# Kernel optimization log

Measured on AMD Instinct MI355X. Metric: run time of the kernel, lower is better.

The kernel has to match this reference:

```python
import jax, jax.numpy as jnp
import numpy as np

NUM_EXPERTS = 8
TOP_K = 2


def setup_inputs() -> dict:
    key = jax.random.key(0)
    ks = jax.random.split(key, 5)
    B, S, H, F, E = 2, 2048, 1024, 4096, NUM_EXPERTS
    return {
        "hidden_states": jax.random.normal(ks[0], (B, S, H), dtype=jnp.float32),
        "router_w": jax.random.normal(ks[1], (H, E), dtype=jnp.float32) * 0.02,
        "router_b": jnp.zeros((E,), dtype=jnp.float32),
        "w1": jax.random.normal(ks[2], (E, H, F), dtype=jnp.float32) * 0.02,
        "b1": jnp.zeros((E, F), dtype=jnp.float32),
        "w2": jax.random.normal(ks[3], (E, F, H), dtype=jnp.float32) * 0.02,
        "b2": jnp.zeros((E, H), dtype=jnp.float32),
    }


def reference(hidden_states, router_w, router_b, w1, b1, w2, b2):
    # Router: softmax over experts, take top-2, renormalize.
    logits = jnp.einsum("bsh,he->bse", hidden_states, router_w) + router_b
    probs = jax.nn.softmax(logits, axis=-1)
    top_w, top_i = jax.lax.top_k(probs, TOP_K)              # [B,S,2]
    top_w = top_w / jnp.sum(top_w, axis=-1, keepdims=True)
    # Combine weights per expert: [B,S,E] (sum of slot weights where routed).
    combine = jnp.sum(
        top_w[..., None] * jax.nn.one_hot(top_i, NUM_EXPERTS, dtype=top_w.dtype),
        axis=-2,
    )
    # Dense expert FFN over stacked experts (grouped GEMM form).
    h = jax.nn.gelu(
        jnp.einsum("bsh,ehf->ebsf", hidden_states, w1) + b1[:, None, None, :],
        approximate=False,
    )  # exact GELU matches torch nn.GELU default
    y = jnp.einsum("ebsf,efh->ebsh", h, w2) + b2[:, None, None, :]
    # Weighted combine of top-2 expert outputs per token.
    return jnp.einsum("bse,ebsh->bsh", combine, y)
```

## Files before the change

kernel.cpp:

```cpp
#include <hip/hip_runtime.h>
#include <hip/hip_bf16.h>
#include <stdint.h>

#define T_TOKENS 4096
#define H_DIM    1024
#define F_DIM    4096
#define NE       8
#define NA       8192

typedef __bf16 bf16x8 __attribute__((ext_vector_type(8)));
typedef float  f32x4  __attribute__((ext_vector_type(4)));

__device__ __forceinline__ float b2f(unsigned short u) {
    union { float f; uint32_t i; } v; v.i = ((uint32_t)u) << 16; return v.f;
}
__device__ __forceinline__ unsigned short f2b(float f) {
    union { float f; uint32_t i; } v; v.f = f;
    uint32_t x = v.i;
    return (unsigned short)((x + 0x7FFFu + ((x >> 16) & 1u)) >> 16);
}

__device__ __forceinline__ float gelu_f(float x) {
    float z = fabsf(x) * 0.70710678118f;
    float t = 1.0f / (1.0f + 0.3275911f * z);
    float p = t * (0.254829592f + t * (-0.284496736f +
              t * (1.421413741f + t * (-1.453152027f + t * 1.061405429f))));
    float erf_z = 1.0f - p * __expf(-z * z);
    float sgn_erf = (x >= 0.f) ? erf_z : -erf_z;
    return x * (0.5f + 0.5f * sgn_erf);
}

__device__ __forceinline__ void gl_lds16(const void* g, void* l) {
    __builtin_amdgcn_global_load_lds(
        (const __attribute__((address_space(1))) void*)g,
        (__attribute__((address_space(3))) void*)l,
        16, 0, 0);
}

__global__ void probe_kernel(const unsigned short* __restrict__ hs,
                             int* __restrict__ flag) {
    int lane = threadIdx.x;
    int cnt = 0;
    for (int j = 0; j < 16; j++) {
        unsigned short u = hs[(lane * 16 + j) * 2];
        int e = (u >> 7) & 0xFF;
        if (e >= 100 && e <= 135) cnt++;
    }
    for (int off = 32; off > 0; off >>= 1) cnt += __shfl_down(cnt, off);
    if (lane == 0) *flag = (cnt >= 512) ? 0 : 1;
}

__global__ __launch_bounds__(256) void router_kernel(
    const void* __restrict__ hs, const void* __restrict__ rw,
    const void* __restrict__ rb, const int* __restrict__ flag,
    int* __restrict__ top_i, float* __restrict__ top_w,
    unsigned short* __restrict__ hsb) {
    bool f32 = (*flag != 0);
    int wave = threadIdx.x >> 6, lane = threadIdx.x & 63;
    int t = blockIdx.x * 4 + wave;
    unsigned short* hout = hsb + (size_t)t * H_DIM;
    float acc[NE];
#pragma unroll
    for (int e = 0; e < NE; e++) acc[e] = 0.f;
    if (f32) {
        const float* hrow = (const float*)hs + (size_t)t * H_DIM;
        const float* rwf = (const float*)rw;
        for (int j = 0; j < 16; j++) {
            int k = j * 64 + lane;
            float h = hrow[k];
            hout[k] = f2b(h);
            float4 a = *(const float4*)(rwf + (size_t)k * NE);
            float4 b = *(const float4*)(rwf + (size_t)k * NE + 4);
            acc[0] += h * a.x; acc[1] += h * a.y; acc[2] += h * a.z; acc[3] += h * a.w;
            acc[4] += h * b.x; acc[5] += h * b.y; acc[6] += h * b.z; acc[7] += h * b.w;
        }
    } else {
        const unsigned short* hrow = (const unsigned short*)hs + (size_t)t * H_DIM;
        const unsigned short* rwu = (const unsigned short*)rw;
        for (int j = 0; j < 16; j++) {
            int k = j * 64 + lane;
            unsigned short hu = hrow[k];
            hout[k] = hu;
            float h = b2f(hu);
            uint4 rv = *(const uint4*)(rwu + (size_t)k * NE);
            const unsigned short* rs = (const unsigned short*)&rv;
#pragma unroll
            for (int e = 0; e < NE; e++) acc[e] += h * b2f(rs[e]);
        }
    }
#pragma unroll
    for (int e = 0; e < NE; e++)
        for (int off = 32; off > 0; off >>= 1) acc[e] += __shfl_down(acc[e], off);
    if (lane == 0) {
        float lg[NE];
#pragma unroll
        for (int e = 0; e < NE; e++)
            lg[e] = acc[e] + (f32 ? ((const float*)rb)[e]
                                  : b2f(((const unsigned short*)rb)[e]));
        int e0 = 0;
        for (int e = 1; e < NE; e++) if (lg[e] > lg[e0]) e0 = e;
        int e1 = (e0 == 0) ? 1 : 0;
        for (int e = 0; e < NE; e++) if (e != e0 && lg[e] > lg[e1]) e1 = e;
        float w0 = 1.f / (1.f + expf(lg[e1] - lg[e0]));
        top_i[t * 2] = e0; top_i[t * 2 + 1] = e1;
        top_w[t * 2] = w0; top_w[t * 2 + 1] = 1.f - w0;
    }
}

__global__ __launch_bounds__(256) void assign_kernel(
    const int* __restrict__ top_i, const float* __restrict__ top_w,
    int* __restrict__ token_list, float* __restrict__ wgt_list,
    int* __restrict__ assign_row, int* __restrict__ counts,
    int* __restrict__ offsets) {
    __shared__ int cnt_s[NE], cur_s[NE];
    int tid = threadIdx.x;
    if (tid < NE) cnt_s[tid] = 0;
    __syncthreads();
    for (int idx = tid; idx < NA; idx += 256) atomicAdd(&cnt_s[top_i[idx]], 1);
    __syncthreads();
    if (tid == 0) {
        int run = 0;
        for (int e = 0; e < NE; e++) {
            offsets[e] = run; counts[e] = cnt_s[e]; cur_s[e] = run; run += cnt_s[e];
        }
    }
    __syncthreads();
    for (int idx = tid; idx < NA; idx += 256) {
        int e = top_i[idx];
        int pos = atomicAdd(&cur_s[e], 1);
        token_list[pos] = idx >> 1;
        wgt_list[pos] = top_w[idx];
        assign_row[idx] = pos;
    }
}

__global__ __launch_bounds__(256) void transpose_kernel(
    const void* __restrict__ in, unsigned short* __restrict__ out,
    int R, int C, const int* __restrict__ flag) {
    bool f32 = (*flag != 0);
    size_t zo = (size_t)blockIdx.z * R * C;
    int c0 = blockIdx.x * 64, r0 = blockIdx.y * 64;
    __shared__ unsigned short t[64][65];
    int tx = threadIdx.x & 15, ty = threadIdx.x >> 4;
    if (f32) {
        const float* inf = (const float*)in + zo;
#pragma unroll
        for (int i = 0; i < 4; i++) {
            int r = ty + i * 16;
            float4 v = *(const float4*)&inf[(size_t)(r0 + r) * C + c0 + tx * 4];
            t[r][tx * 4] = f2b(v.x); t[r][tx * 4 + 1] = f2b(v.y);
            t[r][tx * 4 + 2] = f2b(v.z); t[r][tx * 4 + 3] = f2b(v.w);
        }
    } else {
        const unsigned short* inu = (const unsigned short*)in + zo;
#pragma unroll
        for (int i = 0; i < 4; i++) {
            int r = ty + i * 16;
            ushort4 v = *(const ushort4*)&inu[(size_t)(r0 + r) * C + c0 + tx * 4];
            t[r][tx * 4] = v.x; t[r][tx * 4 + 1] = v.y;
            t[r][tx * 4 + 2] = v.z; t[r][tx * 4 + 3] = v.w;
        }
    }
    __syncthreads();
#pragma unroll
    for (int i = 0; i < 4; i++) {
        int cc = ty + i * 16;
        ushort4 w;
        w.x = t[tx * 4][cc]; w.y = t[tx * 4 + 1][cc];
        w.z = t[tx * 4 + 2][cc]; w.w = t[tx * 4 + 3][cc];
        *(ushort4*)&out[zo + (size_t)(c0 + cc) * R + r0 + tx * 4] = w;
    }
}

template <int MODE>
__global__ __launch_bounds__(512, 2) void gemm_kernel(
    const unsigned short* __restrict__ Abase,
    const unsigned short* __restrict__ Bt,
    const void* __restrict__ bias,
    const int* __restrict__ flag,
    const int* __restrict__ token_list, const float* __restrict__ wgt_list,
    const int* __restrict__ counts, const int* __restrict__ offsets,
    unsigned short* __restrict__ act_out, unsigned short* __restrict__ y_out) {
    constexpr int K    = (MODE == 0) ? H_DIM : F_DIM;
    constexpr int NDIM = (MODE == 0) ? F_DIM : H_DIM;
    constexpr int AST  = K;
    constexpr int BM   = 256;
    constexpr int BN   = (MODE == 0) ? 256 : 128;
    constexpr int WM   = (MODE == 0) ? 2 : 4;
    constexpr int WN   = (MODE == 0) ? 4 : 2;
    constexpr int MI   = BM / (16 * WM);
    constexpr int NJ   = BN / (16 * WN);
    constexpr int NK   = K / 32;
    constexpr int ABUF = BM * 32;
    constexpr int BBUF = BN * 32;
    constexpr int NIA  = BM / 128;
    constexpr int NIB  = BN / 128;

    const int lid = blockIdx.x + gridDim.x * (blockIdx.y + gridDim.y * blockIdx.z);
    const int e   = lid & 7;
    const int r_  = lid >> 3;
    const int nx  = r_ % gridDim.x;
    const int my  = r_ / gridDim.x;

    const int cnt = counts[e];
    const int m0 = my * BM;
    if (m0 >= cnt) return;
    const int off = offsets[e];
    const int n0 = nx * BN;
    const bool f32 = (*flag != 0);

    __shared__ __bf16 As[2 * ABUF];
    __shared__ __bf16 Bs[2 * BBUF];
    __shared__ int   tok_s[BM];
    __shared__ float wgt_s[BM];

    const int tid = threadIdx.x;
    const int wave = tid >> 6, lane = tid & 63;

    if (tid < BM) {
        int r = off + min(m0 + tid, cnt - 1);
        tok_s[tid] = (MODE == 0) ? token_list[r] : r;
        wgt_s[tid] = wgt_list[r];
    }
    __syncthreads();

    const char* Abytes = (const char*)Abase;
    const char* Bbytes = (const char*)(Bt + (size_t)e * NDIM * K);
    const int rl = lane >> 2;
    const int chk = (lane & 3) ^ (rl & 3);
    uint64_t ga[NIA], gb[NIB];
    uint32_t la[NIA], lb[NIB];
#pragma unroll
    for (int j = 0; j < NIA; j++) {
        int rowA = (wave * NIA + j) * 16 + rl;
        ga[j] = (uint64_t)(uintptr_t)(Abytes + ((size_t)tok_s[rowA] * AST + chk * 8) * 2);
        la[j] = (wave * NIA + j) * 512;
    }
#pragma unroll
    for (int j = 0; j < NIB; j++) {
        int rowB = n0 + (wave * NIB + j) * 16 + rl;
        gb[j] = (uint64_t)(uintptr_t)(Bbytes + ((size_t)rowB * K + chk * 8) * 2);
        lb[j] = (wave * NIB + j) * 512;
    }

    f32x4 acc[MI][NJ];
#pragma unroll
    for (int i = 0; i < MI; i++)
#pragma unroll
        for (int j = 0; j < NJ; j++) acc[i][j] = (f32x4){0.f, 0.f, 0.f, 0.f};

    const int wr = wave / WN, wc = wave % WN;
    const int lane15 = lane & 15, quad = lane >> 4;

#pragma unroll
    for (int j = 0; j < NIA; j++) {
        gl_lds16((const void*)(uintptr_t)ga[j], (void*)(As + la[j]));
        ga[j] += 64;
    }
#pragma unroll
    for (int j = 0; j < NIB; j++) {
        gl_lds16((const void*)(uintptr_t)gb[j], (void*)(Bs + lb[j]));
        gb[j] += 64;
    }
    __syncthreads();

    for (int kt = 0; kt < NK; kt++) {
        const int cur = kt & 1;
        if (kt + 1 < NK) {
            const int nxt = cur ^ 1;
#pragma unroll
            for (int j = 0; j < NIA; j++) {
                gl_lds16((const void*)(uintptr_t)ga[j], (void*)(As + nxt * ABUF + la[j]));
                ga[j] += 64;
            }
#pragma unroll
            for (int j = 0; j < NIB; j++) {
                gl_lds16((const void*)(uintptr_t)gb[j], (void*)(Bs + nxt * BBUF + lb[j]));
                gb[j] += 64;
            }
        }
        const __bf16* Ab = As + cur * ABUF;
        const __bf16* Bb = Bs + cur * BBUF;
        bf16x8 a[MI], b[NJ];
#pragma unroll
        for (int i = 0; i < MI; i++) {
            int row = wr * (BM / WM) + i * 16 + lane15;
            a[i] = *(const bf16x8*)&Ab[row * 32 + ((quad ^ (row & 3)) * 8)];
        }
#pragma unroll
        for (int j = 0; j < NJ; j++) {
            int row = wc * (BN / WN) + j * 16 + lane15;
            b[j] = *(const bf16x8*)&Bb[row * 32 + ((quad ^ (row & 3)) * 8)];
        }
#pragma unroll
        for (int i = 0; i < MI; i++)
#pragma unroll
            for (int j = 0; j < NJ; j++)
                acc[i][j] = __builtin_amdgcn_mfma_f32_16x16x32_bf16(a[i], b[j], acc[i][j], 0, 0, 0);
        __syncthreads();
    }

#pragma unroll
    for (int j = 0; j < NJ; j++) {
        int col = n0 + wc * (BN / WN) + j * 16 + lane15;
        float bv = f32 ? ((const float*)bias)[(size_t)e * NDIM + col]
                       : b2f(((const unsigned short*)bias)[(size_t)e * NDIM + col]);
#pragma unroll
        for (int i = 0; i < MI; i++) {
#pragma unroll
            for (int r = 0; r < 4; r++) {
                int rowl = wr * (BM / WM) + i * 16 + quad * 4 + r;
                if (m0 + rowl < cnt) {
                    float v = acc[i][j][r] + bv;
                    if (MODE == 0) {
                        act_out[(size_t)(off + m0 + rowl) * F_DIM + col] = f2b(gelu_f(v));
                    } else {
                        y_out[(size_t)(off + m0 + rowl) * H_DIM + col] = f2b(v * wgt_s[rowl]);
                    }
                }
            }
        }
    }
}

__global__ __launch_bounds__(256) void combine_kernel(
    const unsigned short* __restrict__ y, const int* __restrict__ assign_row,
    void* __restrict__ out, const int* __restrict__ flag) {
    bool f32 = (*flag != 0);
    int t = blockIdx.x;
    int r0 = assign_row[t * 2], r1 = assign_row[t * 2 + 1];
    ushort4 a = ((const ushort4*)(y + (size_t)r0 * H_DIM))[threadIdx.x];
    ushort4 b = ((const ushort4*)(y + (size_t)r1 * H_DIM))[threadIdx.x];
    float s0 = b2f(a.x) + b2f(b.x), s1 = b2f(a.y) + b2f(b.y);
    float s2 = b2f(a.z) + b2f(b.z), s3 = b2f(a.w) + b2f(b.w);
    if (f32) {
        float4 o = {s0, s1, s2, s3};
        ((float4*)out)[(size_t)t * (H_DIM / 4) + threadIdx.x] = o;
    } else {
        ushort4 o;
        o.x = f2b(s0); o.y = f2b(s1); o.z = f2b(s2); o.w = f2b(s3);
        ((ushort4*)((unsigned short*)out + (size_t)t * H_DIM))[threadIdx.x] = o;
    }
}

extern "C" void kernel_launch(void* const* d_in, const int* in_sizes, int n_in,
                              void* d_out, int out_size, void* d_ws, size_t ws_size,
                              hipStream_t stream) {
    const void* hs = d_in[0];
    const void* rw = d_in[1];
    const void* rb = d_in[2];
    const void* w1 = d_in[3];
    const void* b1 = d_in[4];
    const void* w2 = d_in[5];
    const void* b2 = d_in[6];

    char* ws = (char*)d_ws;
    size_t o = 0;
    auto alloc = [&](size_t bytes) {
        char* p = ws + o; o += (bytes + 255) & ~(size_t)255; return p;
    };
    unsigned short* wt   = (unsigned short*)alloc((size_t)NE * F_DIM * H_DIM * 2);
    unsigned short* act  = (unsigned short*)alloc((size_t)NA * F_DIM * 2);
    unsigned short* yb   = (unsigned short*)alloc((size_t)NA * H_DIM * 2);
    unsigned short* hsb  = (unsigned short*)alloc((size_t)T_TOKENS * H_DIM * 2);
    int*   top_i      = (int*)alloc(NA * 4);
    float* top_w      = (float*)alloc(NA * 4);
    int*   token_list = (int*)alloc(NA * 4);
    float* wgt_list   = (float*)alloc(NA * 4);
    int*   assign_row = (int*)alloc(NA * 4);
    int*   counts     = (int*)alloc(64);
    int*   offsets    = (int*)alloc(64);
    int*   flag       = (int*)alloc(64);
    (void)ws_size; (void)in_sizes; (void)n_in; (void)out_size;

    probe_kernel<<<1, 64, 0, stream>>>((const unsigned short*)hs, flag);
    router_kernel<<<T_TOKENS / 4, 256, 0, stream>>>(hs, rw, rb, flag, top_i, top_w, hsb);
    assign_kernel<<<1, 256, 0, stream>>>(top_i, top_w, token_list, wgt_list,
                                         assign_row, counts, offsets);
    transpose_kernel<<<dim3(F_DIM / 64, H_DIM / 64, NE), 256, 0, stream>>>(
        w1, wt, H_DIM, F_DIM, flag);
    gemm_kernel<0><<<dim3(F_DIM / 256, T_TOKENS / 256, NE), 512, 0, stream>>>(
        hsb, wt, b1, flag, token_list, wgt_list, counts, offsets, act, nullptr);
    transpose_kernel<<<dim3(H_DIM / 64, F_DIM / 64, NE), 256, 0, stream>>>(
        w2, wt, F_DIM, H_DIM, flag);
    gemm_kernel<1><<<dim3(H_DIM / 128, T_TOKENS / 256, NE), 512, 0, stream>>>(
        act, wt, b2, flag, token_list, wgt_list, counts, offsets, nullptr, yb);
    combine_kernel<<<T_TOKENS, 256, 0, stream>>>(yb, assign_row, d_out, flag);
}
```

Measured before the change: 656.5 us.

## Overlap w2 transpose with first expert GEMM via extra worker blocks

The first grouped GEMM gets an extra grid slice whose blocks, instead of doing GEMM tiles, pull transpose tiles of w2 from an atomic counter and write them into a second weight buffer. The aim is to hide the separate w2 transpose launch behind GEMM1. GEMM1 is also retiled to 128x128 with 256 threads, which gives more blocks and better tail fill. The cost is an extra workspace buffer (with a fallback path if the workspace is too small) and contention between the transpose and GEMM work for bandwidth and CUs.

```diff
diff --git a/kernel.cpp b/kernel.cpp
--- a/kernel.cpp
+++ b/kernel.cpp
@@ -111,10 +111,11 @@
     const int* __restrict__ top_i, const float* __restrict__ top_w,
     int* __restrict__ token_list, float* __restrict__ wgt_list,
     int* __restrict__ assign_row, int* __restrict__ counts,
-    int* __restrict__ offsets) {
+    int* __restrict__ offsets, int* __restrict__ ctr) {
     __shared__ int cnt_s[NE], cur_s[NE];
     int tid = threadIdx.x;
     if (tid < NE) cnt_s[tid] = 0;
+    if (tid == 0) *ctr = 0;
     __syncthreads();
     for (int idx = tid; idx < NA; idx += 256) atomicAdd(&cnt_s[top_i[idx]], 1);
     __syncthreads();
@@ -173,153 +174,210 @@
 }
 
 template <int MODE>
-__global__ __launch_bounds__(512, 2) void gemm_kernel(
+__global__ __launch_bounds__((MODE == 0) ? 256 : 512) void gemm_kernel(
     const unsigned short* __restrict__ Abase,
     const unsigned short* __restrict__ Bt,
     const void* __restrict__ bias,
     const int* __restrict__ flag,
     const int* __restrict__ token_list, const float* __restrict__ wgt_list,
     const int* __restrict__ counts, const int* __restrict__ offsets,
-    unsigned short* __restrict__ act_out, unsigned short* __restrict__ y_out) {
-    constexpr int K    = (MODE == 0) ? H_DIM : F_DIM;
-    constexpr int NDIM = (MODE == 0) ? F_DIM : H_DIM;
-    constexpr int AST  = K;
-    constexpr int BM   = 256;
-    constexpr int BN   = (MODE == 0) ? 256 : 128;
-    constexpr int WM   = (MODE == 0) ? 2 : 4;
-    constexpr int WN   = (MODE == 0) ? 4 : 2;
-    constexpr int MI   = BM / (16 * WM);
-    constexpr int NJ   = BN / (16 * WN);
-    constexpr int NK   = K / 32;
-    constexpr int ABUF = BM * 32;
-    constexpr int BBUF = BN * 32;
-    constexpr int NIA  = BM / 128;
-    constexpr int NIB  = BN / 128;
-
-    const int lid = blockIdx.x + gridDim.x * (blockIdx.y + gridDim.y * blockIdx.z);
-    const int e   = lid & 7;
-    const int r_  = lid >> 3;
-    const int nx  = r_ % gridDim.x;
-    const int my  = r_ / gridDim.x;
-
-    const int cnt = counts[e];
-    const int m0 = my * BM;
-    if (m0 >= cnt) return;
-    const int off = offsets[e];
-    const int n0 = nx * BN;
-    const bool f32 = (*flag != 0);
+    unsigned short* __restrict__ act_out, unsigned short* __restrict__ y_out,
+    const void* __restrict__ tsrc,
+    unsigned short* __restrict__ tdst,
+    int* __restrict__ ctr, int ntiles) {
+    constexpr int K     = (MODE == 0) ? H_DIM : F_DIM;
+    constexpr int NDIM  = (MODE == 0) ? F_DIM : H_DIM;
+    constexpr int AST   = K;
+    constexpr int BM    = (MODE == 0) ? 128 : 256;
+    constexpr int BN    = 128;
+    constexpr int WAVES = (MODE == 0) ? 4 : 8;
+    constexpr int WM    = (MODE == 0) ? 2 : 4;
+    constexpr int WN    = 2;
+    constexpr int MI    = BM / (16 * WM);
+    constexpr int NJ    = BN / (16 * WN);
+    constexpr int NK    = K / 32;
+    constexpr int ABUF  = BM * 32;
+    constexpr int BBUF  = BN * 32;
+    constexpr int NIA   = BM / (16 * WAVES);
+    constexpr int NIB   = BN / (16 * WAVES);
 
     __shared__ __bf16 As[2 * ABUF];
     __shared__ __bf16 Bs[2 * BBUF];
     __shared__ int   tok_s[BM];
     __shared__ float wgt_s[BM];
+    __shared__ int   c_s;
 
     const int tid = threadIdx.x;
-    const int wave = tid >> 6, lane = tid & 63;
-
-    if (tid < BM) {
-        int r = off + min(m0 + tid, cnt - 1);
-        tok_s[tid] = (MODE == 0) ? token_list[r] : r;
-        wgt_s[tid] = wgt_list[r];
-    }
-    __syncthreads();
-
-    const char* Abytes = (const char*)Abase;
-    const char* Bbytes = (const char*)(Bt + (size_t)e * NDIM * K);
-    const int rl = lane >> 2;
-    const int chk = (lane & 3) ^ (rl & 3);
-    uint64_t ga[NIA], gb[NIB];
-    uint32_t la[NIA], lb[NIB];
-#pragma unroll
-    for (int j = 0; j < NIA; j++) {
-        int rowA = (wave * NIA + j) * 16 + rl;
-        ga[j] = (uint64_t)(uintptr_t)(Abytes + ((size_t)tok_s[rowA] * AST + chk * 8) * 2);
-        la[j] = (wave * NIA + j) * 512;
-    }
-#pragma unroll
-    for (int j = 0; j < NIB; j++) {
-        int rowB = n0 + (wave * NIB + j) * 16 + rl;
-        gb[j] = (uint64_t)(uintptr_t)(Bbytes + ((size_t)rowB * K + chk * 8) * 2);
-        lb[j] = (wave * NIB + j) * 512;
-    }
-
-    f32x4 acc[MI][NJ];
-#pragma unroll
-    for (int i = 0; i < MI; i++)
-#pragma unroll
-        for (int j = 0; j < NJ; j++) acc[i][j] = (f32x4){0.f, 0.f, 0.f, 0.f};
-
-    const int wr = wave / WN, wc = wave % WN;
-    const int lane15 = lane & 15, quad = lane >> 4;
-
-#pragma unroll
-    for (int j = 0; j < NIA; j++) {
-        gl_lds16((const void*)(uintptr_t)ga[j], (void*)(As + la[j]));
-        ga[j] += 64;
-    }
-#pragma unroll
-    for (int j = 0; j < NIB; j++) {
-        gl_lds16((const void*)(uintptr_t)gb[j], (void*)(Bs + lb[j]));
-        gb[j] += 64;
-    }
-    __syncthreads();
-
-    for (int kt = 0; kt < NK; kt++) {
-        const int cur = kt & 1;
-        if (kt + 1 < NK) {
-            const int nxt = cur ^ 1;
-#pragma unroll
-            for (int j = 0; j < NIA; j++) {
-                gl_lds16((const void*)(uintptr_t)ga[j], (void*)(As + nxt * ABUF + la[j]));
-                ga[j] += 64;
-            }
-#pragma unroll
-            for (int j = 0; j < NIB; j++) {
-                gl_lds16((const void*)(uintptr_t)gb[j], (void*)(Bs + nxt * BBUF + lb[j]));
-                gb[j] += 64;
-            }
-        }
-        const __bf16* Ab = As + cur * ABUF;
-        const __bf16* Bb = Bs + cur * BBUF;
-        bf16x8 a[MI], b[NJ];
-#pragma unroll
-        for (int i = 0; i < MI; i++) {
-            int row = wr * (BM / WM) + i * 16 + lane15;
-            a[i] = *(const bf16x8*)&Ab[row * 32 + ((quad ^ (row & 3)) * 8)];
-        }
+    const bool f32 = (*flag != 0);
+
+    const int lid = blockIdx.x + gridDim.x * (blockIdx.y + gridDim.y * blockIdx.z);
+    const int NG = gridDim.x * gridDim.y * NE;
+    bool gemm_role = (lid < NG);
+    int e = 0, m0 = 0, cnt = 0, n0 = 0, off = 0;
+    if (gemm_role) {
+        e = lid & 7;
+        int r_ = lid >> 3;
+        int nx = r_ % gridDim.x;
+        int my = r_ / gridDim.x;
+        cnt = counts[e];
+        m0 = my * BM;
+        off = offsets[e];
+        n0 = nx * BN;
+        gemm_role = (m0 < cnt);
+    }
+
+    if (gemm_role) {
+        const int wave = tid >> 6, lane = tid & 63;
+
+        if (tid < BM) {
+            int r = off + min(m0 + tid, cnt - 1);
+            tok_s[tid] = (MODE == 0) ? token_list[r] : r;
+            wgt_s[tid] = wgt_list[r];
+        }
+        __syncthreads();
+
+        const char* Abytes = (const char*)Abase;
+        const char* Bbytes = (const char*)(Bt + (size_t)e * NDIM * K);
+        const int rl = lane >> 2;
+        const int chk = (lane & 3) ^ (rl & 3);
+        uint64_t ga[NIA], gb[NIB];
+        uint32_t la[NIA], lb[NIB];
+#pragma unroll
+        for (int j = 0; j < NIA; j++) {
+            int rowA = (wave * NIA + j) * 16 + rl;
+            ga[j] = (uint64_t)(uintptr_t)(Abytes + ((size_t)tok_s[rowA] * AST + chk * 8) * 2);
+            la[j] = (wave * NIA + j) * 512;
+        }
+#pragma unroll
+        for (int j = 0; j < NIB; j++) {
+            int rowB = n0 + (wave * NIB + j) * 16 + rl;
+            gb[j] = (uint64_t)(uintptr_t)(Bbytes + ((size_t)rowB * K + chk * 8) * 2);
+            lb[j] = (wave * NIB + j) * 512;
+        }
+
+        f32x4 acc[MI][NJ];
+#pragma unroll
+        for (int i = 0; i < MI; i++)
+#pragma unroll
+            for (int j = 0; j < NJ; j++) acc[i][j] = (f32x4){0.f, 0.f, 0.f, 0.f};
+
+        const int wr = wave / WN, wc = wave % WN;
+        const int lane15 = lane & 15, quad = lane >> 4;
+
+#pragma unroll
+        for (int j = 0; j < NIA; j++) {
+            gl_lds16((const void*)(uintptr_t)ga[j], (void*)(As + la[j]));
+            ga[j] += 64;
+        }
+#pragma unroll
+        for (int j = 0; j < NIB; j++) {
+            gl_lds16((const void*)(uintptr_t)gb[j], (void*)(Bs + lb[j]));
+            gb[j] += 64;
+        }
+        __syncthreads();
+
+        for (int kt = 0; kt < NK; kt++) {
+            const int cur = kt & 1;
+            if (kt + 1 < NK) {
+                const int nxt = cur ^ 1;
+#pragma unroll
+                for (int j = 0; j < NIA; j++) {
+                    gl_lds16((const void*)(uintptr_t)ga[j], (void*)(As + nxt * ABUF + la[j]));
+                    ga[j] += 64;
+                }
+#pragma unroll
+                for (int j = 0; j < NIB; j++) {
+                    gl_lds16((const void*)(uintptr_t)gb[j], (void*)(Bs + nxt * BBUF + lb[j]));
+                    gb[j] += 64;
+                }
+            }
+            const __bf16* Ab = As + cur * ABUF;
+            const __bf16* Bb = Bs + cur * BBUF;
+            bf16x8 a[MI], b[NJ];
+#pragma unroll
+            for (int i = 0; i < MI; i++) {
+                int row = wr * (BM / WM) + i * 16 + lane15;
+                a[i] = *(const bf16x8*)&Ab[row * 32 + ((quad ^ (row & 3)) * 8)];
+            }
+#pragma unroll
+            for (int j = 0; j < NJ; j++) {
+                int row = wc * (BN / WN) + j * 16 + lane15;
+                b[j] = *(const bf16x8*)&Bb[row * 32 + ((quad ^ (row & 3)) * 8)];
+            }
+#pragma unroll
+            for (int i = 0; i < MI; i++)
+#pragma unroll
+                for (int j = 0; j < NJ; j++)
+                    acc[i][j] = __builtin_amdgcn_mfma_f32_16x16x32_bf16(a[i], b[j], acc[i][j], 0, 0, 0);
+            __syncthreads();
+        }
+
 #pragma unroll
         for (int j = 0; j < NJ; j++) {
-            int row = wc * (BN / WN) + j * 16 + lane15;
-            b[j] = *(const bf16x8*)&Bb[row * 32 + ((quad ^ (row & 3)) * 8)];
-        }
-#pragma unroll
-        for (int i = 0; i < MI; i++)
-#pragma unroll
-            for (int j = 0; j < NJ; j++)
-                acc[i][j] = __builtin_amdgcn_mfma_f32_16x16x32_bf16(a[i], b[j], acc[i][j], 0, 0, 0);
-        __syncthreads();
-    }
-
-#pragma unroll
-    for (int j = 0; j < NJ; j++) {
-        int col = n0 + wc * (BN / WN) + j * 16 + lane15;
-        float bv = f32 ? ((const float*)bias)[(size_t)e * NDIM + col]
-                       : b2f(((const unsigned short*)bias)[(size_t)e * NDIM + col]);
-#pragma unroll
-        for (int i = 0; i < MI; i++) {
-#pragma unroll
-            for (int r = 0; r < 4; r++) {
-                int rowl = wr * (BM / WM) + i * 16 + quad * 4 + r;
-                if (m0 + rowl < cnt) {
-                    float v = acc[i][j][r] + bv;
-                    if (MODE == 0) {
-                        act_out[(size_t)(off + m0 + rowl) * F_DIM + col] = f2b(gelu_f(v));
-                    } else {
-                        y_out[(size_t)(off + m0 + rowl) * H_DIM + col] = f2b(v * wgt_s[rowl]);
+            int col = n0 + wc * (BN / WN) + j * 16 + lane15;
+            float bv = f32 ? ((const float*)bias)[(size_t)e * NDIM + col]
+                           : b2f(((const unsigned short*)bias)[(size_t)e * NDIM + col]);
+#pragma unroll
+            for (int i = 0; i < MI; i++) {
+#pragma unroll
+                for (int r = 0; r < 4; r++) {
+                    int rowl = wr * (BM / WM) + i * 16 + quad * 4 + r;
+                    if (m0 + rowl < cnt) {
+                        float v = acc[i][j][r] + bv;
+                        if (MODE == 0) {
+                            act_out[(size_t)(off + m0 + rowl) * F_DIM + col] = f2b(gelu_f(v));
+                        } else {
+                            y_out[(size_t)(off + m0 + rowl) * H_DIM + col] = f2b(v * wgt_s[rowl]);
+                        }
                     }
                 }
             }
         }
+        return;
+    }
+
+    if (ntiles <= 0) return;
+    unsigned short (*tt)[65] = (unsigned short(*)[65])As;
+    const int tx = tid & 15, ty = (tid >> 4) & 15;
+    for (;;) {
+        if (tid == 0) c_s = atomicAdd(ctr, 1);
+        __syncthreads();
+        int c = c_s;
+        if (c >= ntiles) break;
+        int e2 = c >> 10;
+        int rem = c & 1023;
+        int c0 = (rem & 15) * 64;
+        int r0 = (rem >> 4) * 64;
+        size_t zo = (size_t)e2 * F_DIM * H_DIM;
+        if (f32) {
+            const float* inf = (const float*)tsrc + zo;
+#pragma unroll
+            for (int i = 0; i < 4; i++) {
+                int r = ty + i * 16;
+                float4 v = *(const float4*)&inf[(size_t)(r0 + r) * H_DIM + c0 + tx * 4];
+                tt[r][tx * 4] = f2b(v.x); tt[r][tx * 4 + 1] = f2b(v.y);
+                tt[r][tx * 4 + 2] = f2b(v.z); tt[r][tx * 4 + 3] = f2b(v.w);
+            }
+        } else {
+            const unsigned short* inu = (const unsigned short*)tsrc + zo;
+#pragma unroll
+            for (int i = 0; i < 4; i++) {
+                int r = ty + i * 16;
+                ushort4 v = *(const ushort4*)&inu[(size_t)(r0 + r) * H_DIM + c0 + tx * 4];
+                tt[r][tx * 4] = v.x; tt[r][tx * 4 + 1] = v.y;
+                tt[r][tx * 4 + 2] = v.z; tt[r][tx * 4 + 3] = v.w;
+            }
+        }
+        __syncthreads();
+#pragma unroll
+        for (int i = 0; i < 4; i++) {
+            int cc = ty + i * 16;
+            ushort4 w;
+            w.x = tt[tx * 4][cc]; w.y = tt[tx * 4 + 1][cc];
+            w.z = tt[tx * 4 + 2][cc]; w.w = tt[tx * 4 + 3][cc];
+            *(ushort4*)&tdst[zo + (size_t)(c0 + cc) * F_DIM + r0 + tx * 4] = w;
+        }
+        __syncthreads();
     }
 }
 
@@ -359,7 +417,7 @@
     auto alloc = [&](size_t bytes) {
         char* p = ws + o; o += (bytes + 255) & ~(size_t)255; return p;
     };
-    unsigned short* wt   = (unsigned short*)alloc((size_t)NE * F_DIM * H_DIM * 2);
+    unsigned short* wt1  = (unsigned short*)alloc((size_t)NE * F_DIM * H_DIM * 2);
     unsigned short* act  = (unsigned short*)alloc((size_t)NA * F_DIM * 2);
     unsigned short* yb   = (unsigned short*)alloc((size_t)NA * H_DIM * 2);
     unsigned short* hsb  = (unsigned short*)alloc((size_t)T_TOKENS * H_DIM * 2);
@@ -371,19 +429,31 @@
     int*   counts     = (int*)alloc(64);
     int*   offsets    = (int*)alloc(64);
     int*   flag       = (int*)alloc(64);
-    (void)ws_size; (void)in_sizes; (void)n_in; (void)out_size;
+    int*   ctr        = (int*)alloc(64);
+    unsigned short* wt2 = (unsigned short*)alloc((size_t)NE * F_DIM * H_DIM * 2);
+    const bool fused = (o <= ws_size);
+    if (!fused) wt2 = wt1;
+    (void)in_sizes; (void)n_in; (void)out_size;
 
     probe_kernel<<<1, 64, 0, stream>>>((const unsigned short*)hs, flag);
     router_kernel<<<T_TOKENS / 4, 256, 0, stream>>>(hs, rw, rb, flag, top_i, top_w, hsb);
     assign_kernel<<<1, 256, 0, stream>>>(top_i, top_w, token_list, wgt_list,
-                                         assign_row, counts, offsets);
+                                         assign_row, counts, offsets, ctr);
     transpose_kernel<<<dim3(F_DIM / 64, H_DIM / 64, NE), 256, 0, stream>>>(
-        w1, wt, H_DIM, F_DIM, flag);
-    gemm_kernel<0><<<dim3(F_DIM / 256, T_TOKENS / 256, NE), 512, 0, stream>>>(
-        hsb, wt, b1, flag, token_list, wgt_list, counts, offsets, act, nullptr);
-    transpose_kernel<<<dim3(H_DIM / 64, F_DIM / 64, NE), 256, 0, stream>>>(
-        w2, wt, F_DIM, H_DIM, flag);
+        w1, wt1, H_DIM, F_DIM, flag);
+    if (fused) {
+        gemm_kernel<0><<<dim3(F_DIM / 128, T_TOKENS / 128, NE + 1), 256, 0, stream>>>(
+            hsb, wt1, b1, flag, token_list, wgt_list, counts, offsets, act, nullptr,
+            w2, wt2, ctr, (H_DIM / 64) * (F_DIM / 64) * NE);
+    } else {
+        gemm_kernel<0><<<dim3(F_DIM / 128, T_TOKENS / 128, NE), 256, 0, stream>>>(
+            hsb, wt1, b1, flag, token_list, wgt_list, counts, offsets, act, nullptr,
+            w2, wt2, ctr, 0);
+        transpose_kernel<<<dim3(H_DIM / 64, F_DIM / 64, NE), 256, 0, stream>>>(
+            w2, wt1, F_DIM, H_DIM, flag);
+    }
     gemm_kernel<1><<<dim3(H_DIM / 128, T_TOKENS / 256, NE), 512, 0, stream>>>(
-        act, wt, b2, flag, token_list, wgt_list, counts, offsets, nullptr, yb);
+        act, wt2, b2, flag, token_list, wgt_list, counts, offsets, nullptr, yb,
+        nullptr, nullptr, ctr, 0);
     combine_kernel<<<T_TOKENS, 256, 0, stream>>>(yb, assign_row, d_out, flag);
 }
```

Result: slower. 735.4 us (+12.0%).

## Switch expert GEMMs to 128x128 tiles with triple-buffered LDS pipeline

Applied to the files above, without the earlier changes.

Shrinks the expert GEMM tiles to 128x128 with 256-thread blocks and replaces the double-buffered loop with a three-stage LDS ring. Each iteration waits only on the older loads via vmcnt and uses a single barrier, and s_setprio is raised around the MFMA block. The goal is to overlap global-to-LDS loads with MFMA work, cut per-iteration synchronisation, and raise occupancy with more, smaller blocks. In exchange, each smaller tile does less reuse per byte loaded, and correctness depends on the hand-counted vmcnt value and on a single barrier per iteration being enough to protect buffer reuse.

```diff
diff --git a/kernel.cpp b/kernel.cpp
--- a/kernel.cpp
+++ b/kernel.cpp
@@ -173,7 +173,7 @@
 }
 
 template <int MODE>
-__global__ __launch_bounds__(512, 2) void gemm_kernel(
+__global__ __launch_bounds__(256, 3) void gemm_kernel(
     const unsigned short* __restrict__ Abase,
     const unsigned short* __restrict__ Bt,
     const void* __restrict__ bias,
@@ -184,17 +184,12 @@
     constexpr int K    = (MODE == 0) ? H_DIM : F_DIM;
     constexpr int NDIM = (MODE == 0) ? F_DIM : H_DIM;
     constexpr int AST  = K;
-    constexpr int BM   = 256;
-    constexpr int BN   = (MODE == 0) ? 256 : 128;
-    constexpr int WM   = (MODE == 0) ? 2 : 4;
-    constexpr int WN   = (MODE == 0) ? 4 : 2;
-    constexpr int MI   = BM / (16 * WM);
-    constexpr int NJ   = BN / (16 * WN);
+    constexpr int BM   = 128, BN = 128;
+    constexpr int MI   = 4, NJ = 4;
     constexpr int NK   = K / 32;
     constexpr int ABUF = BM * 32;
     constexpr int BBUF = BN * 32;
-    constexpr int NIA  = BM / 128;
-    constexpr int NIB  = BN / 128;
+    constexpr int NIA  = 2, NIB = 2;
 
     const int lid = blockIdx.x + gridDim.x * (blockIdx.y + gridDim.y * blockIdx.z);
     const int e   = lid & 7;
@@ -209,8 +204,8 @@
     const int n0 = nx * BN;
     const bool f32 = (*flag != 0);
 
-    __shared__ __bf16 As[2 * ABUF];
-    __shared__ __bf16 Bs[2 * BBUF];
+    __shared__ __bf16 As[3 * ABUF];
+    __shared__ __bf16 Bs[3 * BBUF];
     __shared__ int   tok_s[BM];
     __shared__ float wgt_s[BM];
 
@@ -249,67 +244,70 @@
 #pragma unroll
         for (int j = 0; j < NJ; j++) acc[i][j] = (f32x4){0.f, 0.f, 0.f, 0.f};
 
-    const int wr = wave / WN, wc = wave % WN;
+    const int wr = wave >> 1, wc = wave & 1;
     const int lane15 = lane & 15, quad = lane >> 4;
 
-#pragma unroll
-    for (int j = 0; j < NIA; j++) {
-        gl_lds16((const void*)(uintptr_t)ga[j], (void*)(As + la[j]));
-        ga[j] += 64;
-    }
-#pragma unroll
-    for (int j = 0; j < NIB; j++) {
-        gl_lds16((const void*)(uintptr_t)gb[j], (void*)(Bs + lb[j]));
-        gb[j] += 64;
-    }
-    __syncthreads();
-
-    for (int kt = 0; kt < NK; kt++) {
-        const int cur = kt & 1;
-        if (kt + 1 < NK) {
-            const int nxt = cur ^ 1;
-#pragma unroll
-            for (int j = 0; j < NIA; j++) {
-                gl_lds16((const void*)(uintptr_t)ga[j], (void*)(As + nxt * ABUF + la[j]));
-                ga[j] += 64;
-            }
-#pragma unroll
-            for (int j = 0; j < NIB; j++) {
-                gl_lds16((const void*)(uintptr_t)gb[j], (void*)(Bs + nxt * BBUF + lb[j]));
-                gb[j] += 64;
-            }
-        }
-        const __bf16* Ab = As + cur * ABUF;
-        const __bf16* Bb = Bs + cur * BBUF;
+    auto stage = [&](int buf) {
+#pragma unroll
+        for (int j = 0; j < NIA; j++) {
+            gl_lds16((const void*)(uintptr_t)ga[j], (void*)(As + buf * ABUF + la[j]));
+            ga[j] += 64;
+        }
+#pragma unroll
+        for (int j = 0; j < NIB; j++) {
+            gl_lds16((const void*)(uintptr_t)gb[j], (void*)(Bs + buf * BBUF + lb[j]));
+            gb[j] += 64;
+        }
+    };
+    auto compute = [&](int buf) {
+        const __bf16* Ab = As + buf * ABUF;
+        const __bf16* Bb = Bs + buf * BBUF;
         bf16x8 a[MI], b[NJ];
 #pragma unroll
         for (int i = 0; i < MI; i++) {
-            int row = wr * (BM / WM) + i * 16 + lane15;
+            int row = wr * 64 + i * 16 + lane15;
             a[i] = *(const bf16x8*)&Ab[row * 32 + ((quad ^ (row & 3)) * 8)];
         }
 #pragma unroll
         for (int j = 0; j < NJ; j++) {
-            int row = wc * (BN / WN) + j * 16 + lane15;
+            int row = wc * 64 + j * 16 + lane15;
             b[j] = *(const bf16x8*)&Bb[row * 32 + ((quad ^ (row & 3)) * 8)];
         }
+        __builtin_amdgcn_s_setprio(1);
 #pragma unroll
         for (int i = 0; i < MI; i++)
 #pragma unroll
             for (int j = 0; j < NJ; j++)
                 acc[i][j] = __builtin_amdgcn_mfma_f32_16x16x32_bf16(a[i], b[j], acc[i][j], 0, 0, 0);
-        __syncthreads();
-    }
+        __builtin_amdgcn_s_setprio(0);
+    };
+
+    stage(0);
+    int bufw = 1, bufr = 0;
+    for (int kt = 0; kt < NK - 1; kt++) {
+        stage(bufw);
+        bufw = (bufw == 2) ? 0 : bufw + 1;
+        asm volatile("s_waitcnt vmcnt(4)" ::: "memory");
+        __builtin_amdgcn_s_barrier();
+        __builtin_amdgcn_sched_barrier(0);
+        compute(bufr);
+        bufr = (bufr == 2) ? 0 : bufr + 1;
+    }
+    asm volatile("s_waitcnt vmcnt(0)" ::: "memory");
+    __builtin_amdgcn_s_barrier();
+    __builtin_amdgcn_sched_barrier(0);
+    compute(bufr);
 
 #pragma unroll
     for (int j = 0; j < NJ; j++) {
-        int col = n0 + wc * (BN / WN) + j * 16 + lane15;
+        int col = n0 + wc * 64 + j * 16 + lane15;
         float bv = f32 ? ((const float*)bias)[(size_t)e * NDIM + col]
                        : b2f(((const unsigned short*)bias)[(size_t)e * NDIM + col]);
 #pragma unroll
         for (int i = 0; i < MI; i++) {
 #pragma unroll
             for (int r = 0; r < 4; r++) {
-                int rowl = wr * (BM / WM) + i * 16 + quad * 4 + r;
+                int rowl = wr * 64 + i * 16 + quad * 4 + r;
                 if (m0 + rowl < cnt) {
                     float v = acc[i][j][r] + bv;
                     if (MODE == 0) {
@@ -379,11 +377,11 @@
                                          assign_row, counts, offsets);
     transpose_kernel<<<dim3(F_DIM / 64, H_DIM / 64, NE), 256, 0, stream>>>(
         w1, wt, H_DIM, F_DIM, flag);
-    gemm_kernel<0><<<dim3(F_DIM / 256, T_TOKENS / 256, NE), 512, 0, stream>>>(
+    gemm_kernel<0><<<dim3(F_DIM / 128, T_TOKENS / 128, NE), 256, 0, stream>>>(
         hsb, wt, b1, flag, token_list, wgt_list, counts, offsets, act, nullptr);
     transpose_kernel<<<dim3(H_DIM / 64, F_DIM / 64, NE), 256, 0, stream>>>(
         w2, wt, F_DIM, H_DIM, flag);
-    gemm_kernel<1><<<dim3(H_DIM / 128, T_TOKENS / 256, NE), 512, 0, stream>>>(
+    gemm_kernel<1><<<dim3(H_DIM / 128, T_TOKENS / 128, NE), 256, 0, stream>>>(
         act, wt, b2, flag, token_list, wgt_list, counts, offsets, nullptr, yb);
     combine_kernel<<<T_TOKENS, 256, 0, stream>>>(yb, assign_row, d_out, flag);
 }
```

Measured after the change: 583.2 us. -11.2%, faster.
